# Kernel tuning notes

Measured on AMD Instinct MI355X. Metric: run time of the kernel, lower is better.

The kernel has to match this reference:

```python
import jax, jax.numpy as jnp
import numpy as np

NUM_HEADS = 4
TEMPERATURE = 1.0
EDGE_WEIGHT = 0.5


def setup_inputs() -> dict:
    key = jax.random.key(0)
    k1, k2, k3 = jax.random.split(key, 3)
    x = jax.random.normal(k1, (4, 2048, 512), dtype=jnp.float32)
    gate_w = jax.random.normal(k2, (1, 1), dtype=jnp.float32)
    gate_b = jax.random.normal(k3, (1,), dtype=jnp.float32)
    return {"x": x, "gate_w": gate_w, "gate_b": gate_b}


def _forward(x, gate_w, gate_b):
    B, N, C = x.shape
    H = NUM_HEADS
    hd = C // H
    # F.normalize(x, dim=-1) with eps=1e-12
    norm = jnp.linalg.norm(x, axis=-1, keepdims=True)
    x_norm = x / jnp.maximum(norm, 1e-12)
    # multi-head cosine-sim attention
    xh = x_norm.reshape(B, N, H, hd).transpose(0, 2, 1, 3)  # (B,H,N,hd)
    sim = jnp.einsum("bhnd,bhmd->bhnm", xh, xh) / (hd ** 0.5 * TEMPERATURE)
    attn = jax.nn.softmax(sim, axis=-1)
    xv = x.reshape(B, N, H, hd).transpose(0, 2, 1, 3)  # (B,H,N,hd)
    x_refined = jnp.einsum("bhnm,bhmd->bhnd", attn, xv)
    x_refined = x_refined.transpose(0, 2, 1, 3).reshape(B, N, C)
    # edge-variance mask (no_grad in torch -> stop_gradient)
    diff = jnp.var(x, axis=-1, keepdims=True, ddof=1)  # (B,N,1), unbiased like torch
    edge_mask = jax.nn.sigmoid((diff - diff.mean()) / (jnp.std(diff, ddof=1) + 1e-6))
    edge_mask = jax.lax.stop_gradient(edge_mask)
    x_refined = (1.0 + EDGE_WEIGHT * edge_mask) * x_refined
    # scalar gate: Linear(1,1) + Sigmoid on global mean
    gate_input = x.mean(axis=1, keepdims=True).mean(axis=-1, keepdims=True)  # (B,1,1)
    gate = jax.nn.sigmoid(gate_input * gate_w[0, 0] + gate_b[0])
    x_refined = gate * x_refined
    return x + x_refined


def reference(x, gate_w, gate_b):
    return _forward(x, gate_w, gate_b)
```

## Files before the change

### kernel.cpp

```cpp
#include <hip/hip_runtime.h>
#include <stdint.h>

#define B_   4
#define N_   2048
#define C_   512
#define H_   4
#define HD_  128
#define BN_  (B_ * N_)
#define NIT_ 32
#define SCALE_LOG2E 0.1275129727595311f

typedef __attribute__((ext_vector_type(8))) short  short8;
typedef __attribute__((ext_vector_type(4))) unsigned short ushort4_t;
typedef __attribute__((ext_vector_type(4))) float  float4_t;
typedef __attribute__((ext_vector_type(8))) __bf16 bf16x8;

static __device__ __forceinline__ unsigned short f2bf(float f) {
  union { float f; uint32_t u; } v; v.f = f;
  uint32_t r = v.u + 0x7FFFu + ((v.u >> 16) & 1u);
  return (unsigned short)(r >> 16);
}

static __device__ __forceinline__ uint32_t cvtpk_bf16(float lo, float hi) {
  uint32_t r;
  asm("v_cvt_pk_bf16_f32 %0, %1, %2" : "=v"(r) : "v"(lo), "v"(hi));
  return r;
}

#if __has_builtin(__builtin_amdgcn_exp2f)
#define EXP2(x) __builtin_amdgcn_exp2f(x)
#else
#define EXP2(x) exp2f(x)
#endif

static __device__ __forceinline__ float4_t mfma16(short8 a, short8 b, float4_t c) {
  return __builtin_amdgcn_mfma_f32_16x16x32_bf16(
      __builtin_bit_cast(bf16x8, a), __builtin_bit_cast(bf16x8, b), c, 0, 0, 0);
}

#define GLOAD16(SRC, DST)                                               \
  __builtin_amdgcn_global_load_lds(                                     \
      (const __attribute__((address_space(1))) void*)(SRC),             \
      (__attribute__((address_space(3))) void*)(DST), 16, 0, 0)

__global__ __launch_bounds__(256) void k_stats(
    const float* __restrict__ x, unsigned short* __restrict__ xnq,
    float* __restrict__ diff, float* __restrict__ toksum) {
  int tok  = blockIdx.x * 4 + (threadIdx.x >> 6);
  int lane = threadIdx.x & 63;
  const float* xr = x + (size_t)tok * C_;
  float4_t a = *(const float4_t*)(xr + lane * 8);
  float4_t b = *(const float4_t*)(xr + lane * 8 + 4);
  float s = 0.f, ss = 0.f;
#pragma unroll
  for (int j = 0; j < 4; ++j) {
    s  += a[j] + b[j];
    ss += a[j] * a[j] + b[j] * b[j];
  }
#pragma unroll
  for (int o = 1; o < 64; o <<= 1) {
    s  += __shfl_xor(s, o);
    ss += __shfl_xor(ss, o);
  }
  float rn = 1.f / fmaxf(sqrtf(ss), 1e-12f);
  short8 o8;
#pragma unroll
  for (int j = 0; j < 4; ++j) {
    o8[j]     = (short)f2bf(a[j] * rn);
    o8[j + 4] = (short)f2bf(b[j] * rn);
  }
  *(short8*)(xnq + (size_t)tok * C_ + lane * 8) = o8;
  if (lane == 0) {
    diff[tok]   = (ss - s * s * (1.f / C_)) * (1.f / (C_ - 1));
    toksum[tok] = s;
  }
}

__global__ __launch_bounds__(256) void k_transpose(
    const float* __restrict__ x, unsigned short* __restrict__ xvT) {
  __shared__ float tr[HD_][65];
  int bh = blockIdx.x & 15, nt = blockIdx.x >> 4;
  int b = bh >> 2, h = bh & 3;
  int n0 = nt * 64, c0 = h * HD_;
  int t = threadIdx.x;
  int dm = (t & 31) * 4;
  int nr = t >> 5;
#pragma unroll
  for (int p = 0; p < 8; ++p) {
    int n = p * 8 + nr;
    float4_t v = *(const float4_t*)(x + ((size_t)(b * N_ + n0 + n)) * C_ + c0 + dm);
#pragma unroll
    for (int k = 0; k < 4; ++k) tr[dm + k][n] = v[k];
  }
  __syncthreads();
#pragma unroll
  for (int p4 = 0; p4 < 4; ++p4) {
    int c = p4 * 256 + t;
    int d = c >> 3, pb = c & 7;
    int lg = pb ^ (d & 7);
    int kbase = 32 * (lg >> 2) + 4 * (lg & 3);
    short8 o8;
#pragma unroll
    for (int e = 0; e < 8; ++e)
      o8[e] = (short)f2bf(tr[d][kbase + 16 * (e >> 2) + (e & 3)]);
    *(short8*)(xvT + ((size_t)(bh * HD_ + d)) * N_ + n0 + pb * 8) = o8;
  }
}

__global__ __launch_bounds__(256) void k_finalize(
    const float* __restrict__ diff, const float* __restrict__ toksum,
    const float* __restrict__ gw, const float* __restrict__ gb,
    float* __restrict__ stats) {
  __shared__ float sh[4][8];
  int t = threadIdx.x, l = t & 63, w = t >> 6;
  float s1 = 0.f, s2 = 0.f;
  for (int i = t; i < BN_; i += 256) { float d = diff[i]; s1 += d; s2 += d * d; }
  float bs0 = 0.f, bs1 = 0.f, bs2 = 0.f, bs3 = 0.f;
  for (int i = t; i < N_; i += 256) {
    bs0 += toksum[i];          bs1 += toksum[N_ + i];
    bs2 += toksum[2 * N_ + i]; bs3 += toksum[3 * N_ + i];
  }
#pragma unroll
  for (int o = 1; o < 64; o <<= 1) {
    s1 += __shfl_xor(s1, o);  s2 += __shfl_xor(s2, o);
    bs0 += __shfl_xor(bs0, o); bs1 += __shfl_xor(bs1, o);
    bs2 += __shfl_xor(bs2, o); bs3 += __shfl_xor(bs3, o);
  }
  if (l == 0) {
    sh[w][0] = s1; sh[w][1] = s2;
    sh[w][2] = bs0; sh[w][3] = bs1; sh[w][4] = bs2; sh[w][5] = bs3;
  }
  __syncthreads();
  if (t == 0) {
    float S1 = sh[0][0] + sh[1][0] + sh[2][0] + sh[3][0];
    float S2 = sh[0][1] + sh[1][1] + sh[2][1] + sh[3][1];
    float mean = S1 / (float)BN_;
    float var  = (S2 - S1 * S1 / (float)BN_) / (float)(BN_ - 1);
    float rstd = 1.f / (sqrtf(var) + 1e-6f);
    stats[0] = mean; stats[1] = rstd;
    float w00 = gw[0], bb = gb[0];
#pragma unroll
    for (int q = 0; q < 4; ++q) {
      float bsum = sh[0][2 + q] + sh[1][2 + q] + sh[2][2 + q] + sh[3][2 + q];
      float gi = bsum / (float)(N_ * C_);
      stats[2 + q] = 1.f / (1.f + __expf(-(gi * w00 + bb)));
    }
  }
}

__global__ __launch_bounds__(128, 1) void k_attn(
    const float* __restrict__ x, const unsigned short* __restrict__ xnq,
    const unsigned short* __restrict__ xvT, const float* __restrict__ diff,
    const float* __restrict__ stats, float* __restrict__ out) {
  __shared__ unsigned short sm[16384];
  int i  = blockIdx.x;
  int bh = ((i & 7) << 1) | ((i >> 3) & 1);
  int qt = i >> 4;
  int b = bh >> 2, h = bh & 3, c0 = h * HD_;
  int tid = threadIdx.x, w = tid >> 6, l = tid & 63;
  int g = l >> 4, r = l & 15;
  int q0 = qt * 64;

  short8 qf[4][4];
  const unsigned short* qbase = xnq + ((size_t)(b * N_ + q0)) * C_ + c0;
#pragma unroll
  for (int qs = 0; qs < 4; ++qs)
#pragma unroll
    for (int cs = 0; cs < 4; ++cs)
      qf[qs][cs] = *(const short8*)(qbase + (size_t)(qs * 16 + r) * C_ + g * 8 + cs * 32);

  short8 kf[2][4];
  auto loadK = [&](int it) {
    const unsigned short* kb =
        xnq + ((size_t)(b * N_ + it * 64 + w * 32 + r)) * C_ + c0 + g * 8;
#pragma unroll
    for (int ks = 0; ks < 2; ++ks)
#pragma unroll
      for (int cs = 0; cs < 4; ++cs)
        kf[ks][cs] = *(const short8*)(kb + ks * 16 * C_ + cs * 32);
  };

  auto stageV = [&](int it, int cb) {
    const unsigned short* vsrc =
        xvT + ((size_t)(bh * HD_ + w * 64 + (l >> 3))) * N_ + it * 64 + (l & 7) * 8;
    unsigned short* vdst = &sm[cb * 8192 + w * 4096];
#pragma unroll
    for (int j = 0; j < 8; ++j)
      GLOAD16(vsrc + (size_t)j * 8 * N_, vdst + j * 512);
  };

  float4_t acc[8][4];
  float ls[4] = {0.f, 0.f, 0.f, 0.f};
#pragma unroll
  for (int dt = 0; dt < 8; ++dt)
#pragma unroll
    for (int qs = 0; qs < 4; ++qs) acc[dt][qs] = (float4_t){0.f, 0.f, 0.f, 0.f};

  int vre = r * 64 + (((w * 4 + g) ^ (r & 7)) * 8);

  loadK(0);
  stageV(0, 0);
  __syncthreads();

#pragma unroll 2
  for (int it = 0; it < NIT_; ++it) {
    int cb = it & 1;
    if (it + 1 < NIT_) stageV(it + 1, cb ^ 1);

    float4_t p[2][4];
#pragma unroll
    for (int ks = 0; ks < 2; ++ks)
#pragma unroll
      for (int qs = 0; qs < 4; ++qs) p[ks][qs] = (float4_t){0.f, 0.f, 0.f, 0.f};

    __builtin_amdgcn_s_setprio(1);
#pragma unroll
    for (int ks = 0; ks < 2; ++ks)
#pragma unroll
      for (int cs = 0; cs < 4; ++cs) {
        short8 kfr = kf[ks][cs];
#pragma unroll
        for (int qs = 0; qs < 4; ++qs)
          p[ks][qs] = mfma16(kfr, qf[qs][cs], p[ks][qs]);
      }
    __builtin_amdgcn_s_setprio(0);

    if (it + 1 < NIT_) loadK(it + 1);

    union { short8 s8; uint32_t u[4]; } pfq[4];
#pragma unroll
    for (int ks = 0; ks < 2; ++ks)
#pragma unroll
      for (int qs = 0; qs < 4; ++qs) {
        float e0 = EXP2(p[ks][qs][0] * SCALE_LOG2E);
        float e1 = EXP2(p[ks][qs][1] * SCALE_LOG2E);
        float e2 = EXP2(p[ks][qs][2] * SCALE_LOG2E);
        float e3 = EXP2(p[ks][qs][3] * SCALE_LOG2E);
        ls[qs] += (e0 + e1) + (e2 + e3);
        pfq[qs].u[ks * 2 + 0] = cvtpk_bf16(e0, e1);
        pfq[qs].u[ks * 2 + 1] = cvtpk_bf16(e2, e3);
      }

    __builtin_amdgcn_s_setprio(1);
#pragma unroll
    for (int dt = 0; dt < 8; ++dt) {
      short8 vf = *(const short8*)(&sm[cb * 8192 + dt * 1024 + vre]);
#pragma unroll
      for (int qs = 0; qs < 4; ++qs)
        acc[dt][qs] = mfma16(vf, pfq[qs].s8, acc[dt][qs]);
    }
    __builtin_amdgcn_s_setprio(0);
    __syncthreads();
  }

#pragma unroll
  for (int qs = 0; qs < 4; ++qs) {
    ls[qs] += __shfl_xor(ls[qs], 16);
    ls[qs] += __shfl_xor(ls[qs], 32);
  }
  float* smf = (float*)sm;
  if (g == 0) {
#pragma unroll
    for (int qs = 0; qs < 4; ++qs) smf[w * 64 + qs * 16 + r] = ls[qs];
  }
  __syncthreads();
  float lst[4];
#pragma unroll
  for (int qs = 0; qs < 4; ++qs)
    lst[qs] = smf[qs * 16 + r] + smf[64 + qs * 16 + r];
  __syncthreads();

  float4_t* ex = (float4_t*)sm;
  if (w == 0) {
#pragma unroll
    for (int k = 0; k < 4; ++k)
#pragma unroll
      for (int qs = 0; qs < 4; ++qs)
        ex[l * 16 + ((k * 4 + qs) ^ (l & 15))] = acc[4 + k][qs];
  } else {
#pragma unroll
    for (int k = 0; k < 4; ++k)
#pragma unroll
      for (int qs = 0; qs < 4; ++qs)
        ex[1024 + l * 16 + ((k * 4 + qs) ^ (l & 15))] = acc[k][qs];
  }
  __syncthreads();
  if (w == 0) {
#pragma unroll
    for (int k = 0; k < 4; ++k)
#pragma unroll
      for (int qs = 0; qs < 4; ++qs) {
        float4_t o = ex[1024 + l * 16 + ((k * 4 + qs) ^ (l & 15))];
#pragma unroll
        for (int j = 0; j < 4; ++j) acc[k][qs][j] += o[j];
      }
  } else {
#pragma unroll
    for (int k = 0; k < 4; ++k)
#pragma unroll
      for (int qs = 0; qs < 4; ++qs) {
        float4_t o = ex[l * 16 + ((k * 4 + qs) ^ (l & 15))];
#pragma unroll
        for (int j = 0; j < 4; ++j) acc[4 + k][qs][j] += o[j];
      }
  }

  float mean = stats[0], rstd = stats[1], gate = stats[2 + b];
#pragma unroll
  for (int qs = 0; qs < 4; ++qs) {
    int q = q0 + qs * 16 + r;
    float dv = diff[b * N_ + q];
    float em = 1.f / (1.f + __expf(-(dv - mean) * rstd));
    float f  = gate * (1.f + 0.5f * em) / lst[qs];
    const float* xr = x + ((size_t)(b * N_ + q)) * C_;
    float* orow = out + ((size_t)(b * N_ + q)) * C_;
    if (w == 0) {
#pragma unroll
      for (int k = 0; k < 4; ++k) {
        int dcol = c0 + k * 16 + g * 4;
        float4_t xin = *(const float4_t*)(xr + dcol);
        float4_t o;
#pragma unroll
        for (int j = 0; j < 4; ++j) o[j] = xin[j] + f * acc[k][qs][j];
        *(float4_t*)(orow + dcol) = o;
      }
    } else {
#pragma unroll
      for (int k = 0; k < 4; ++k) {
        int dcol = c0 + (4 + k) * 16 + g * 4;
        float4_t xin = *(const float4_t*)(xr + dcol);
        float4_t o;
#pragma unroll
        for (int j = 0; j < 4; ++j) o[j] = xin[j] + f * acc[4 + k][qs][j];
        *(float4_t*)(orow + dcol) = o;
      }
    }
  }
}

extern "C" void kernel_launch(void* const* d_in, const int* in_sizes, int n_in,
                              void* d_out, int out_size, void* d_ws, size_t ws_size,
                              hipStream_t stream) {
  (void)in_sizes; (void)n_in; (void)out_size; (void)ws_size;
  const float* x  = (const float*)d_in[0];
  const float* gw = (const float*)d_in[1];
  const float* gb = (const float*)d_in[2];
  float* out = (float*)d_out;
  unsigned short* xnq = (unsigned short*)d_ws;
  unsigned short* xvT = xnq + (size_t)BN_ * C_;
  float* diff   = (float*)(xvT + (size_t)BN_ * C_);
  float* toksum = diff + BN_;
  float* stats  = toksum + BN_;
  hipLaunchKernelGGL(k_stats, dim3(BN_ / 4), dim3(256), 0, stream, x, xnq, diff, toksum);
  hipLaunchKernelGGL(k_transpose, dim3(512), dim3(256), 0, stream, x, xvT);
  hipLaunchKernelGGL(k_finalize, dim3(1), dim3(256), 0, stream, diff, toksum, gw, gb, stats);
  hipLaunchKernelGGL(k_attn, dim3(512), dim3(128), 0, stream, x, xnq, xvT, diff, stats, out);
}
```

Baseline: 77.19 us.

## Share staged K/V tiles in LDS across eight waves per 128-query block

The attention kernel now launches 256 blocks of 512 threads, each covering 128 queries. Eight waves split the work into four query groups of 32 and two key halves, so each wave handles fewer queries. K tiles are staged cooperatively into swizzled LDS alongside V, instead of each wave loading K straight from global memory into registers. This cuts redundant global K/V traffic and lowers per-wave register pressure. The costs are more LDS reads and double the LDS footprint, fewer blocks than CUs, and a cross-wave reduction where only half the waves write outputs.

```diff
diff --git a/kernel.cpp b/kernel.cpp
--- a/kernel.cpp
+++ b/kernel.cpp
@@ -148,105 +148,115 @@
   }
 }
 
-__global__ __launch_bounds__(128, 1) void k_attn(
+__global__ __launch_bounds__(512, 1) void k_attn(
     const float* __restrict__ x, const unsigned short* __restrict__ xnq,
     const unsigned short* __restrict__ xvT, const float* __restrict__ diff,
     const float* __restrict__ stats, float* __restrict__ out) {
-  __shared__ unsigned short sm[16384];
+  __shared__ unsigned short sm[32768];
   int i  = blockIdx.x;
   int bh = ((i & 7) << 1) | ((i >> 3) & 1);
   int qt = i >> 4;
   int b = bh >> 2, h = bh & 3, c0 = h * HD_;
   int tid = threadIdx.x, w = tid >> 6, l = tid & 63;
+  int kh = w & 1, qh = w >> 1;
   int g = l >> 4, r = l & 15;
-  int q0 = qt * 64;
-
-  short8 qf[4][4];
+  int q0 = qt * 128 + qh * 32;
+
+  short8 qf[2][4];
   const unsigned short* qbase = xnq + ((size_t)(b * N_ + q0)) * C_ + c0;
 #pragma unroll
-  for (int qs = 0; qs < 4; ++qs)
+  for (int qs = 0; qs < 2; ++qs)
 #pragma unroll
     for (int cs = 0; cs < 4; ++cs)
       qf[qs][cs] = *(const short8*)(qbase + (size_t)(qs * 16 + r) * C_ + g * 8 + cs * 32);
 
-  short8 kf[2][4];
-  auto loadK = [&](int it) {
-    const unsigned short* kb =
-        xnq + ((size_t)(b * N_ + it * 64 + w * 32 + r)) * C_ + c0 + g * 8;
-#pragma unroll
-    for (int ks = 0; ks < 2; ++ks)
-#pragma unroll
-      for (int cs = 0; cs < 4; ++cs)
-        kf[ks][cs] = *(const short8*)(kb + ks * 16 * C_ + cs * 32);
+  const char* smb = (const char*)sm;
+  int kaddr[4];
+#pragma unroll
+  for (int cs = 0; cs < 4; ++cs)
+    kaddr[cs] = (kh * 32 + r) * 256 + (((g * 8 + cs * 32) ^ (r * 8)) * 2);
+  int vaddr = 32768 + r * 128 + (((kh * 4 + g) ^ (r & 7)) * 16);
+
+  float4_t acc[8][2];
+  float ls[2] = {0.f, 0.f};
+#pragma unroll
+  for (int dt = 0; dt < 8; ++dt)
+#pragma unroll
+    for (int qs = 0; qs < 2; ++qs) acc[dt][qs] = (float4_t){0.f, 0.f, 0.f, 0.f};
+
+  auto stage = [&](int it, int cb) {
+    const unsigned short* ks = xnq + ((size_t)(b * N_ + it * 64)) * C_ + c0;
+    unsigned short* kd = &sm[cb * 8192];
+#pragma unroll
+    for (int jj = 0; jj < 2; ++jj) {
+      int j = w * 2 + jj;
+      int row = 4 * j + g;
+      int ssl = r ^ (row & 15);
+      GLOAD16(ks + (size_t)row * C_ + ssl * 8, kd + j * 512 + 0);
+    }
+    const unsigned short* vs = xvT + ((size_t)bh * HD_) * N_ + it * 64;
+    unsigned short* vd = &sm[16384 + cb * 8192];
+#pragma unroll
+    for (int jj = 0; jj < 2; ++jj) {
+      int j = w * 2 + jj;
+      int d = 8 * j + (l >> 3);
+      GLOAD16(vs + (size_t)d * N_ + (l & 7) * 8, vd + j * 512);
+    }
   };
 
-  auto stageV = [&](int it, int cb) {
-    const unsigned short* vsrc =
-        xvT + ((size_t)(bh * HD_ + w * 64 + (l >> 3))) * N_ + it * 64 + (l & 7) * 8;
-    unsigned short* vdst = &sm[cb * 8192 + w * 4096];
-#pragma unroll
-    for (int j = 0; j < 8; ++j)
-      GLOAD16(vsrc + (size_t)j * 8 * N_, vdst + j * 512);
-  };
-
-  float4_t acc[8][4];
-  float ls[4] = {0.f, 0.f, 0.f, 0.f};
-#pragma unroll
-  for (int dt = 0; dt < 8; ++dt)
-#pragma unroll
-    for (int qs = 0; qs < 4; ++qs) acc[dt][qs] = (float4_t){0.f, 0.f, 0.f, 0.f};
-
-  int vre = r * 64 + (((w * 4 + g) ^ (r & 7)) * 8);
-
-  loadK(0);
-  stageV(0, 0);
+  stage(0, 0);
   __syncthreads();
 
 #pragma unroll 2
   for (int it = 0; it < NIT_; ++it) {
     int cb = it & 1;
-    if (it + 1 < NIT_) stageV(it + 1, cb ^ 1);
-
-    float4_t p[2][4];
-#pragma unroll
-    for (int ks = 0; ks < 2; ++ks)
-#pragma unroll
-      for (int qs = 0; qs < 4; ++qs) p[ks][qs] = (float4_t){0.f, 0.f, 0.f, 0.f};
+    if (it + 1 < NIT_) stage(it + 1, cb ^ 1);
+
+    short8 kf[2][4];
+#pragma unroll
+    for (int ks2 = 0; ks2 < 2; ++ks2)
+#pragma unroll
+      for (int cs = 0; cs < 4; ++cs)
+        kf[ks2][cs] = *(const short8*)(smb + kaddr[cs] + cb * 16384 + ks2 * 4096);
+
+    float4_t p[2][2];
+#pragma unroll
+    for (int ks2 = 0; ks2 < 2; ++ks2)
+#pragma unroll
+      for (int qs = 0; qs < 2; ++qs) p[ks2][qs] = (float4_t){0.f, 0.f, 0.f, 0.f};
 
     __builtin_amdgcn_s_setprio(1);
 #pragma unroll
-    for (int ks = 0; ks < 2; ++ks)
+    for (int ks2 = 0; ks2 < 2; ++ks2)
 #pragma unroll
       for (int cs = 0; cs < 4; ++cs) {
-        short8 kfr = kf[ks][cs];
-#pragma unroll
-        for (int qs = 0; qs < 4; ++qs)
-          p[ks][qs] = mfma16(kfr, qf[qs][cs], p[ks][qs]);
+        short8 kfr = kf[ks2][cs];
+#pragma unroll
+        for (int qs = 0; qs < 2; ++qs)
+          p[ks2][qs] = mfma16(kfr, qf[qs][cs], p[ks2][qs]);
       }
     __builtin_amdgcn_s_setprio(0);
 
-    if (it + 1 < NIT_) loadK(it + 1);
-
-    union { short8 s8; uint32_t u[4]; } pfq[4];
-#pragma unroll
-    for (int ks = 0; ks < 2; ++ks)
-#pragma unroll
-      for (int qs = 0; qs < 4; ++qs) {
-        float e0 = EXP2(p[ks][qs][0] * SCALE_LOG2E);
-        float e1 = EXP2(p[ks][qs][1] * SCALE_LOG2E);
-        float e2 = EXP2(p[ks][qs][2] * SCALE_LOG2E);
-        float e3 = EXP2(p[ks][qs][3] * SCALE_LOG2E);
+    union { short8 s8; uint32_t u[4]; } pfq[2];
+#pragma unroll
+    for (int ks2 = 0; ks2 < 2; ++ks2)
+#pragma unroll
+      for (int qs = 0; qs < 2; ++qs) {
+        float e0 = EXP2(p[ks2][qs][0] * SCALE_LOG2E);
+        float e1 = EXP2(p[ks2][qs][1] * SCALE_LOG2E);
+        float e2 = EXP2(p[ks2][qs][2] * SCALE_LOG2E);
+        float e3 = EXP2(p[ks2][qs][3] * SCALE_LOG2E);
         ls[qs] += (e0 + e1) + (e2 + e3);
-        pfq[qs].u[ks * 2 + 0] = cvtpk_bf16(e0, e1);
-        pfq[qs].u[ks * 2 + 1] = cvtpk_bf16(e2, e3);
+        pfq[qs].u[ks2 * 2 + 0] = cvtpk_bf16(e0, e1);
+        pfq[qs].u[ks2 * 2 + 1] = cvtpk_bf16(e2, e3);
       }
 
     __builtin_amdgcn_s_setprio(1);
 #pragma unroll
     for (int dt = 0; dt < 8; ++dt) {
-      short8 vf = *(const short8*)(&sm[cb * 8192 + dt * 1024 + vre]);
-#pragma unroll
-      for (int qs = 0; qs < 4; ++qs)
+      short8 vf = *(const short8*)(smb + vaddr + cb * 16384 + dt * 2048);
+#pragma unroll
+      for (int qs = 0; qs < 2; ++qs)
         acc[dt][qs] = mfma16(vf, pfq[qs].s8, acc[dt][qs]);
     }
     __builtin_amdgcn_s_setprio(0);
@@ -254,84 +264,56 @@
   }
 
 #pragma unroll
-  for (int qs = 0; qs < 4; ++qs) {
+  for (int qs = 0; qs < 2; ++qs) {
     ls[qs] += __shfl_xor(ls[qs], 16);
     ls[qs] += __shfl_xor(ls[qs], 32);
   }
   float* smf = (float*)sm;
   if (g == 0) {
-#pragma unroll
-    for (int qs = 0; qs < 4; ++qs) smf[w * 64 + qs * 16 + r] = ls[qs];
-  }
-  __syncthreads();
-  float lst[4];
-#pragma unroll
-  for (int qs = 0; qs < 4; ++qs)
-    lst[qs] = smf[qs * 16 + r] + smf[64 + qs * 16 + r];
+    smf[w * 16 + r]       = ls[0];
+    smf[128 + w * 16 + r] = ls[1];
+  }
+  __syncthreads();
+  float lst[2];
+  lst[0] = smf[(qh * 2) * 16 + r]       + smf[(qh * 2 + 1) * 16 + r];
+  lst[1] = smf[128 + (qh * 2) * 16 + r] + smf[128 + (qh * 2 + 1) * 16 + r];
   __syncthreads();
 
   float4_t* ex = (float4_t*)sm;
-  if (w == 0) {
-#pragma unroll
-    for (int k = 0; k < 4; ++k)
-#pragma unroll
-      for (int qs = 0; qs < 4; ++qs)
-        ex[l * 16 + ((k * 4 + qs) ^ (l & 15))] = acc[4 + k][qs];
-  } else {
-#pragma unroll
-    for (int k = 0; k < 4; ++k)
-#pragma unroll
-      for (int qs = 0; qs < 4; ++qs)
-        ex[1024 + l * 16 + ((k * 4 + qs) ^ (l & 15))] = acc[k][qs];
-  }
-  __syncthreads();
-  if (w == 0) {
-#pragma unroll
-    for (int k = 0; k < 4; ++k)
-#pragma unroll
-      for (int qs = 0; qs < 4; ++qs) {
-        float4_t o = ex[1024 + l * 16 + ((k * 4 + qs) ^ (l & 15))];
-#pragma unroll
-        for (int j = 0; j < 4; ++j) acc[k][qs][j] += o[j];
+  if (kh == 1) {
+#pragma unroll
+    for (int dt = 0; dt < 8; ++dt)
+#pragma unroll
+      for (int qs = 0; qs < 2; ++qs)
+        ex[(qh * 64 + l) * 16 + ((dt * 2 + qs) ^ (l & 15))] = acc[dt][qs];
+  }
+  __syncthreads();
+  if (kh == 0) {
+#pragma unroll
+    for (int dt = 0; dt < 8; ++dt)
+#pragma unroll
+      for (int qs = 0; qs < 2; ++qs) {
+        float4_t o = ex[(qh * 64 + l) * 16 + ((dt * 2 + qs) ^ (l & 15))];
+#pragma unroll
+        for (int j = 0; j < 4; ++j) acc[dt][qs][j] += o[j];
       }
-  } else {
-#pragma unroll
-    for (int k = 0; k < 4; ++k)
-#pragma unroll
-      for (int qs = 0; qs < 4; ++qs) {
-        float4_t o = ex[l * 16 + ((k * 4 + qs) ^ (l & 15))];
-#pragma unroll
-        for (int j = 0; j < 4; ++j) acc[4 + k][qs][j] += o[j];
-      }
-  }
-
-  float mean = stats[0], rstd = stats[1], gate = stats[2 + b];
-#pragma unroll
-  for (int qs = 0; qs < 4; ++qs) {
-    int q = q0 + qs * 16 + r;
-    float dv = diff[b * N_ + q];
-    float em = 1.f / (1.f + __expf(-(dv - mean) * rstd));
-    float f  = gate * (1.f + 0.5f * em) / lst[qs];
-    const float* xr = x + ((size_t)(b * N_ + q)) * C_;
-    float* orow = out + ((size_t)(b * N_ + q)) * C_;
-    if (w == 0) {
-#pragma unroll
-      for (int k = 0; k < 4; ++k) {
-        int dcol = c0 + k * 16 + g * 4;
+
+    float mean = stats[0], rstd = stats[1], gate = stats[2 + b];
+#pragma unroll
+    for (int qs = 0; qs < 2; ++qs) {
+      int q = q0 + qs * 16 + r;
+      float dv = diff[b * N_ + q];
+      float em = 1.f / (1.f + __expf(-(dv - mean) * rstd));
+      float f  = gate * (1.f + 0.5f * em) / lst[qs];
+      const float* xr = x + ((size_t)(b * N_ + q)) * C_;
+      float* orow = out + ((size_t)(b * N_ + q)) * C_;
+#pragma unroll
+      for (int dt = 0; dt < 8; ++dt) {
+        int dcol = c0 + dt * 16 + g * 4;
         float4_t xin = *(const float4_t*)(xr + dcol);
         float4_t o;
 #pragma unroll
-        for (int j = 0; j < 4; ++j) o[j] = xin[j] + f * acc[k][qs][j];
-        *(float4_t*)(orow + dcol) = o;
-      }
-    } else {
-#pragma unroll
-      for (int k = 0; k < 4; ++k) {
-        int dcol = c0 + (4 + k) * 16 + g * 4;
-        float4_t xin = *(const float4_t*)(xr + dcol);
-        float4_t o;
-#pragma unroll
-        for (int j = 0; j < 4; ++j) o[j] = xin[j] + f * acc[4 + k][qs][j];
+        for (int j = 0; j < 4; ++j) o[j] = xin[j] + f * acc[dt][qs][j];
         *(float4_t*)(orow + dcol) = o;
       }
     }
@@ -354,5 +336,5 @@
   hipLaunchKernelGGL(k_stats, dim3(BN_ / 4), dim3(256), 0, stream, x, xnq, diff, toksum);
   hipLaunchKernelGGL(k_transpose, dim3(512), dim3(256), 0, stream, x, xvT);
   hipLaunchKernelGGL(k_finalize, dim3(1), dim3(256), 0, stream, diff, toksum, gw, gb, stats);
-  hipLaunchKernelGGL(k_attn, dim3(512), dim3(128), 0, stream, x, xnq, xvT, diff, stats, out);
-}
+  hipLaunchKernelGGL(k_attn, dim3(256), dim3(512), 0, stream, x, xnq, xvT, diff, stats, out);
+}
```

Result: faster. 67.10 us (-13.1%).

## Stage K and V tiles in swizzled LDS with 8-wave blocks sharing keys

Applied to the files above, without the earlier changes.

The attention kernel now uses 512-thread blocks covering 128 queries, with eight waves split into two query halves and four key-slice groups. Each iteration stages a 128-key tile of both K and V into double-buffered dynamic shared memory (128 KB) using XOR-swizzled direct global-to-LDS loads, instead of each wave loading K fragments into registers. The final reduction of partial accumulators across key groups goes through LDS in four rounds, and the V transpose layout is changed to match the new swizzle. This targets redundant K global loads and the register pressure of per-wave K fragments. It costs a larger LDS footprint, a four-way cross-wave reduction and fewer, larger blocks (256).

```diff
diff --git a/kernel.cpp b/kernel.cpp
--- a/kernel.cpp
+++ b/kernel.cpp
@@ -7,11 +7,10 @@
 #define H_   4
 #define HD_  128
 #define BN_  (B_ * N_)
-#define NIT_ 32
+#define NIT_ 16
 #define SCALE_LOG2E 0.1275129727595311f
 
 typedef __attribute__((ext_vector_type(8))) short  short8;
-typedef __attribute__((ext_vector_type(4))) unsigned short ushort4_t;
 typedef __attribute__((ext_vector_type(4))) float  float4_t;
 typedef __attribute__((ext_vector_type(8))) __bf16 bf16x8;
 
@@ -96,14 +95,13 @@
 #pragma unroll
   for (int p4 = 0; p4 < 4; ++p4) {
     int c = p4 * 256 + t;
-    int d = c >> 3, pb = c & 7;
-    int lg = pb ^ (d & 7);
+    int d = c >> 3, lg = c & 7;
     int kbase = 32 * (lg >> 2) + 4 * (lg & 3);
     short8 o8;
 #pragma unroll
     for (int e = 0; e < 8; ++e)
       o8[e] = (short)f2bf(tr[d][kbase + 16 * (e >> 2) + (e & 3)]);
-    *(short8*)(xvT + ((size_t)(bh * HD_ + d)) * N_ + n0 + pb * 8) = o8;
+    *(short8*)(xvT + ((size_t)(bh * HD_ + d)) * N_ + n0 + lg * 8) = o8;
   }
 }
 
@@ -148,18 +146,19 @@
   }
 }
 
-__global__ __launch_bounds__(128, 1) void k_attn(
+__global__ __launch_bounds__(512, 2) void k_attn(
     const float* __restrict__ x, const unsigned short* __restrict__ xnq,
     const unsigned short* __restrict__ xvT, const float* __restrict__ diff,
     const float* __restrict__ stats, float* __restrict__ out) {
-  __shared__ unsigned short sm[16384];
+  extern __shared__ unsigned char smraw[];
   int i  = blockIdx.x;
   int bh = ((i & 7) << 1) | ((i >> 3) & 1);
   int qt = i >> 4;
   int b = bh >> 2, h = bh & 3, c0 = h * HD_;
   int tid = threadIdx.x, w = tid >> 6, l = tid & 63;
+  int ks = w & 3, qh = w >> 2;
   int g = l >> 4, r = l & 15;
-  int q0 = qt * 64;
+  int q0 = qt * 128 + qh * 64;
 
   short8 qf[4][4];
   const unsigned short* qbase = xnq + ((size_t)(b * N_ + q0)) * C_ + c0;
@@ -167,27 +166,27 @@
   for (int qs = 0; qs < 4; ++qs)
 #pragma unroll
     for (int cs = 0; cs < 4; ++cs)
-      qf[qs][cs] = *(const short8*)(qbase + (size_t)(qs * 16 + r) * C_ + g * 8 + cs * 32);
-
-  short8 kf[2][4];
-  auto loadK = [&](int it) {
-    const unsigned short* kb =
-        xnq + ((size_t)(b * N_ + it * 64 + w * 32 + r)) * C_ + c0 + g * 8;
-#pragma unroll
-    for (int ks = 0; ks < 2; ++ks)
-#pragma unroll
-      for (int cs = 0; cs < 4; ++cs)
-        kf[ks][cs] = *(const short8*)(kb + ks * 16 * C_ + cs * 32);
-  };
-
-  auto stageV = [&](int it, int cb) {
-    const unsigned short* vsrc =
-        xvT + ((size_t)(bh * HD_ + w * 64 + (l >> 3))) * N_ + it * 64 + (l & 7) * 8;
-    unsigned short* vdst = &sm[cb * 8192 + w * 4096];
-#pragma unroll
-    for (int j = 0; j < 8; ++j)
-      GLOAD16(vsrc + (size_t)j * 8 * N_, vdst + j * 512);
-  };
+      qf[qs][cs] = *(const short8*)(qbase + (size_t)(qs * 16 + r) * C_ + cs * 32 + g * 8);
+
+  uint32_t koff[4], voff[4];
+  const unsigned short* kqbase = xnq + (size_t)b * N_ * C_ + c0;
+  const unsigned short* vgbase = xvT + (size_t)bh * HD_ * N_;
+#pragma unroll
+  for (int jj = 0; jj < 4; ++jj) {
+    int j   = w * 4 + jj;
+    int row = 4 * j + (l >> 4);
+    int cb  = (l & 15) ^ (row & 15);
+    koff[jj] = (uint32_t)(((row >> 5) * 512 + (row & 31)) * C_ + cb * 8);
+    int d   = row;
+    int ksg = (l & 15) ^ (d & 15);
+    voff[jj] = (uint32_t)(d * N_ + (ksg >> 2) * 512 + (ksg & 3) * 8);
+  }
+
+  int kaddr[4];
+#pragma unroll
+  for (int cs = 0; cs < 4; ++cs)
+    kaddr[cs] = (ks * 32 + r) * 256 + (((g + cs * 4) ^ r) * 16);
+  int vaddr = 65536 + r * 256 + (((ks * 4 + g) ^ r) * 16);
 
   float4_t acc[8][4];
   float ls[4] = {0.f, 0.f, 0.f, 0.f};
@@ -196,55 +195,61 @@
 #pragma unroll
     for (int qs = 0; qs < 4; ++qs) acc[dt][qs] = (float4_t){0.f, 0.f, 0.f, 0.f};
 
-  int vre = r * 64 + (((w * 4 + g) ^ (r & 7)) * 8);
-
-  loadK(0);
-  stageV(0, 0);
+  auto stage = [&](int cb) {
+#pragma unroll
+    for (int jj = 0; jj < 4; ++jj)
+      GLOAD16(kqbase + koff[jj], smraw + cb * 32768 + (w * 4 + jj) * 1024);
+#pragma unroll
+    for (int jj = 0; jj < 4; ++jj)
+      GLOAD16(vgbase + voff[jj], smraw + 65536 + cb * 32768 + (w * 4 + jj) * 1024);
+  };
+  auto advance = [&]() {
+#pragma unroll
+    for (int jj = 0; jj < 4; ++jj) { koff[jj] += 32 * C_; voff[jj] += 32; }
+  };
+
+  stage(0);
+  advance();
   __syncthreads();
 
 #pragma unroll 2
   for (int it = 0; it < NIT_; ++it) {
     int cb = it & 1;
-    if (it + 1 < NIT_) stageV(it + 1, cb ^ 1);
-
-    float4_t p[2][4];
-#pragma unroll
-    for (int ks = 0; ks < 2; ++ks)
-#pragma unroll
-      for (int qs = 0; qs < 4; ++qs) p[ks][qs] = (float4_t){0.f, 0.f, 0.f, 0.f};
+    if (it + 1 < NIT_) { stage(cb ^ 1); advance(); }
+
+    const char* smb = (const char*)smraw;
+    union { short8 s8; uint32_t u[4]; } pfq[4];
+
+#pragma unroll
+    for (int ks2 = 0; ks2 < 2; ++ks2) {
+      float4_t p[4];
+#pragma unroll
+      for (int qs = 0; qs < 4; ++qs) p[qs] = (float4_t){0.f, 0.f, 0.f, 0.f};
+      __builtin_amdgcn_s_setprio(1);
+#pragma unroll
+      for (int cs = 0; cs < 4; ++cs) {
+        short8 kfr = *(const short8*)(smb + cb * 32768 + ks2 * 4096 + kaddr[cs]);
+#pragma unroll
+        for (int qs = 0; qs < 4; ++qs)
+          p[qs] = mfma16(kfr, qf[qs][cs], p[qs]);
+      }
+      __builtin_amdgcn_s_setprio(0);
+#pragma unroll
+      for (int qs = 0; qs < 4; ++qs) {
+        float e0 = EXP2(p[qs][0] * SCALE_LOG2E);
+        float e1 = EXP2(p[qs][1] * SCALE_LOG2E);
+        float e2 = EXP2(p[qs][2] * SCALE_LOG2E);
+        float e3 = EXP2(p[qs][3] * SCALE_LOG2E);
+        ls[qs] += (e0 + e1) + (e2 + e3);
+        pfq[qs].u[ks2 * 2 + 0] = cvtpk_bf16(e0, e1);
+        pfq[qs].u[ks2 * 2 + 1] = cvtpk_bf16(e2, e3);
+      }
+    }
 
     __builtin_amdgcn_s_setprio(1);
 #pragma unroll
-    for (int ks = 0; ks < 2; ++ks)
-#pragma unroll
-      for (int cs = 0; cs < 4; ++cs) {
-        short8 kfr = kf[ks][cs];
-#pragma unroll
-        for (int qs = 0; qs < 4; ++qs)
-          p[ks][qs] = mfma16(kfr, qf[qs][cs], p[ks][qs]);
-      }
-    __builtin_amdgcn_s_setprio(0);
-
-    if (it + 1 < NIT_) loadK(it + 1);
-
-    union { short8 s8; uint32_t u[4]; } pfq[4];
-#pragma unroll
-    for (int ks = 0; ks < 2; ++ks)
-#pragma unroll
-      for (int qs = 0; qs < 4; ++qs) {
-        float e0 = EXP2(p[ks][qs][0] * SCALE_LOG2E);
-        float e1 = EXP2(p[ks][qs][1] * SCALE_LOG2E);
-        float e2 = EXP2(p[ks][qs][2] * SCALE_LOG2E);
-        float e3 = EXP2(p[ks][qs][3] * SCALE_LOG2E);
-        ls[qs] += (e0 + e1) + (e2 + e3);
-        pfq[qs].u[ks * 2 + 0] = cvtpk_bf16(e0, e1);
-        pfq[qs].u[ks * 2 + 1] = cvtpk_bf16(e2, e3);
-      }
-
-    __builtin_amdgcn_s_setprio(1);
-#pragma unroll
     for (int dt = 0; dt < 8; ++dt) {
-      short8 vf = *(const short8*)(&sm[cb * 8192 + dt * 1024 + vre]);
+      short8 vf = *(const short8*)(smb + cb * 32768 + dt * 4096 + vaddr);
 #pragma unroll
       for (int qs = 0; qs < 4; ++qs)
         acc[dt][qs] = mfma16(vf, pfq[qs].s8, acc[dt][qs]);
@@ -258,81 +263,61 @@
     ls[qs] += __shfl_xor(ls[qs], 16);
     ls[qs] += __shfl_xor(ls[qs], 32);
   }
-  float* smf = (float*)sm;
-  if (g == 0) {
-#pragma unroll
-    for (int qs = 0; qs < 4; ++qs) smf[w * 64 + qs * 16 + r] = ls[qs];
+  float* lsx = (float*)smraw;
+  if (l < 16) {
+#pragma unroll
+    for (int qs = 0; qs < 4; ++qs) lsx[(w * 4 + qs) * 16 + l] = ls[qs];
   }
   __syncthreads();
   float lst[4];
 #pragma unroll
   for (int qs = 0; qs < 4; ++qs)
-    lst[qs] = smf[qs * 16 + r] + smf[64 + qs * 16 + r];
-  __syncthreads();
-
-  float4_t* ex = (float4_t*)sm;
-  if (w == 0) {
-#pragma unroll
-    for (int k = 0; k < 4; ++k)
-#pragma unroll
-      for (int qs = 0; qs < 4; ++qs)
-        ex[l * 16 + ((k * 4 + qs) ^ (l & 15))] = acc[4 + k][qs];
-  } else {
-#pragma unroll
-    for (int k = 0; k < 4; ++k)
-#pragma unroll
-      for (int qs = 0; qs < 4; ++qs)
-        ex[1024 + l * 16 + ((k * 4 + qs) ^ (l & 15))] = acc[k][qs];
-  }
-  __syncthreads();
-  if (w == 0) {
-#pragma unroll
-    for (int k = 0; k < 4; ++k)
-#pragma unroll
-      for (int qs = 0; qs < 4; ++qs) {
-        float4_t o = ex[1024 + l * 16 + ((k * 4 + qs) ^ (l & 15))];
-#pragma unroll
-        for (int j = 0; j < 4; ++j) acc[k][qs][j] += o[j];
-      }
-  } else {
-#pragma unroll
-    for (int k = 0; k < 4; ++k)
-#pragma unroll
-      for (int qs = 0; qs < 4; ++qs) {
-        float4_t o = ex[l * 16 + ((k * 4 + qs) ^ (l & 15))];
-#pragma unroll
-        for (int j = 0; j < 4; ++j) acc[4 + k][qs][j] += o[j];
-      }
-  }
+    lst[qs] = lsx[((qh * 4 + 0) * 4 + qs) * 16 + r] + lsx[((qh * 4 + 1) * 4 + qs) * 16 + r] +
+              lsx[((qh * 4 + 2) * 4 + qs) * 16 + r] + lsx[((qh * 4 + 3) * 4 + qs) * 16 + r];
 
   float mean = stats[0], rstd = stats[1], gate = stats[2 + b];
+  float fq[4];
 #pragma unroll
   for (int qs = 0; qs < 4; ++qs) {
     int q = q0 + qs * 16 + r;
     float dv = diff[b * N_ + q];
     float em = 1.f / (1.f + __expf(-(dv - mean) * rstd));
-    float f  = gate * (1.f + 0.5f * em) / lst[qs];
-    const float* xr = x + ((size_t)(b * N_ + q)) * C_;
-    float* orow = out + ((size_t)(b * N_ + q)) * C_;
-    if (w == 0) {
-#pragma unroll
-      for (int k = 0; k < 4; ++k) {
-        int dcol = c0 + k * 16 + g * 4;
-        float4_t xin = *(const float4_t*)(xr + dcol);
-        float4_t o;
-#pragma unroll
-        for (int j = 0; j < 4; ++j) o[j] = xin[j] + f * acc[k][qs][j];
-        *(float4_t*)(orow + dcol) = o;
-      }
-    } else {
-#pragma unroll
-      for (int k = 0; k < 4; ++k) {
-        int dcol = c0 + (4 + k) * 16 + g * 4;
-        float4_t xin = *(const float4_t*)(xr + dcol);
-        float4_t o;
-#pragma unroll
-        for (int j = 0; j < 4; ++j) o[j] = xin[j] + f * acc[4 + k][qs][j];
-        *(float4_t*)(orow + dcol) = o;
+    fq[qs] = gate * (1.f + 0.5f * em) / lst[qs];
+  }
+
+  float4_t* ex = (float4_t*)(smraw + 4096);
+#pragma unroll
+  for (int rr = 0; rr < 4; ++rr) {
+    __syncthreads();
+#pragma unroll
+    for (int dd = 0; dd < 2; ++dd)
+#pragma unroll
+      for (int qs = 0; qs < 4; ++qs)
+        ex[((w * 2 + dd) * 4 + qs) * 64 + l] = acc[rr * 2 + dd][qs];
+    __syncthreads();
+    if (ks == rr) {
+#pragma unroll
+      for (int dd = 0; dd < 2; ++dd) {
+        int dt = rr * 2 + dd;
+#pragma unroll
+        for (int qs = 0; qs < 4; ++qs) {
+          float4_t sum = ex[(((qh * 4 + 0) * 2 + dd) * 4 + qs) * 64 + l];
+#pragma unroll
+          for (int k2 = 1; k2 < 4; ++k2) {
+            float4_t o = ex[(((qh * 4 + k2) * 2 + dd) * 4 + qs) * 64 + l];
+#pragma unroll
+            for (int j = 0; j < 4; ++j) sum[j] += o[j];
+          }
+          int q = q0 + qs * 16 + r;
+          int dcol = c0 + dt * 16 + g * 4;
+          const float* xr2 = x + ((size_t)(b * N_ + q)) * C_ + dcol;
+          float* orow = out + ((size_t)(b * N_ + q)) * C_ + dcol;
+          float4_t xin = *(const float4_t*)xr2;
+          float4_t o;
+#pragma unroll
+          for (int j = 0; j < 4; ++j) o[j] = xin[j] + fq[qs] * sum[j];
+          *(float4_t*)orow = o;
+        }
       }
     }
   }
@@ -351,8 +336,11 @@
   float* diff   = (float*)(xvT + (size_t)BN_ * C_);
   float* toksum = diff + BN_;
   float* stats  = toksum + BN_;
+  hipFuncSetAttribute((const void*)k_attn,
+                      hipFuncAttributeMaxDynamicSharedMemorySize, 131072);
   hipLaunchKernelGGL(k_stats, dim3(BN_ / 4), dim3(256), 0, stream, x, xnq, diff, toksum);
   hipLaunchKernelGGL(k_transpose, dim3(512), dim3(256), 0, stream, x, xvT);
   hipLaunchKernelGGL(k_finalize, dim3(1), dim3(256), 0, stream, diff, toksum, gw, gb, stats);
-  hipLaunchKernelGGL(k_attn, dim3(512), dim3(128), 0, stream, x, xnq, xvT, diff, stats, out);
-}
+  hipLaunchKernelGGL(k_attn, dim3(256), dim3(512), 131072, stream,
+                     x, xnq, xvT, diff, stats, out);
+}
```

Measured after the change: 162.6 us. +110.7%, slower.
